# Kernel optimization log

Measured on AMD Instinct MI355X. Metric: run time of the kernel, lower is better.

## Reference

```python
import jax, jax.numpy as jnp
import numpy as np

B, N, C, H, P = 8, 4096, 256, 4, 64  # batch, tokens, hidden, heads, proj_size


def setup_inputs() -> dict:
    key = jax.random.key(0)
    ks = jax.random.split(key, 6)
    sc = 0.02
    x = jax.random.normal(ks[0], (B, N, C), jnp.float32)
    bank = jax.random.normal(ks[1], (B, N, C), jnp.float32)  # unused by forward, kept for fidelity
    W_qkvv = jax.random.normal(ks[2], (4 * C, C), jnp.float32) * sc  # Linear(C, 4C), no bias
    W_E = jax.random.normal(ks[3], (P, N), jnp.float32) * sc          # E = F shared Linear(N, P)
    b_E = jnp.zeros((P,), jnp.float32)
    temperature = jnp.ones((H, 1, 1), jnp.float32)
    temperature2 = jnp.ones((H, 1, 1), jnp.float32)
    W_out1 = jax.random.normal(ks[4], (C // 2, C), jnp.float32) * sc  # out_proj (spatial branch)
    b_out1 = jnp.zeros((C // 2,), jnp.float32)
    W_out2 = jax.random.normal(ks[5], (C // 2, C), jnp.float32) * sc  # out_proj2 (channel branch)
    b_out2 = jnp.zeros((C // 2,), jnp.float32)
    prelu_a = jnp.array(0.25, jnp.float32)  # nn.PReLU() default: single shared slope
    return {"x": x, "bank": bank, "W_qkvv": W_qkvv, "W_E": W_E, "b_E": b_E,
            "temperature": temperature, "temperature2": temperature2,
            "W_out1": W_out1, "b_out1": b_out1, "W_out2": W_out2, "b_out2": b_out2,
            "prelu_a": prelu_a}


def _l2norm(t):
    # torch F.normalize(dim=-1): x / max(||x||_2, eps)
    return t / jnp.maximum(jnp.linalg.norm(t, axis=-1, keepdims=True), 1e-12)


def reference(x, bank, W_qkvv, W_E, b_E, temperature, temperature2,
              W_out1, b_out1, W_out2, b_out2, prelu_a):
    Bb, Nn, Cc = x.shape
    Hh = temperature.shape[0]
    d = Cc // Hh
    # qkvv projection -> [4, B, H, N, d], then transpose token/feature axes -> [B, H, d, N]
    qkvv = (x @ W_qkvv.T).reshape(Bb, Nn, 4, Hh, d).transpose(2, 0, 3, 1, 4)
    q, k, v_ca, v_sa = (qkvv[0].transpose(0, 1, 3, 2), qkvv[1].transpose(0, 1, 3, 2),
                        qkvv[2].transpose(0, 1, 3, 2), qkvv[3].transpose(0, 1, 3, 2))
    # shared linear E=F projects the token axis N -> P (applied to UNnormalized k, v_sa)
    k_proj = jnp.einsum('bhdn,pn->bhdp', k, W_E) + b_E      # [B,H,d,P]
    v_sa_proj = jnp.einsum('bhdn,pn->bhdp', v_sa, W_E) + b_E  # [B,H,d,P]
    qn = _l2norm(q)
    kn = _l2norm(k)
    # channel attention: [B,H,d,d]
    attn_ca = jax.nn.softmax(jnp.einsum('bhdn,bhen->bhde', qn, kn) * temperature, axis=-1)
    x_ca = jnp.einsum('bhde,bhen->bhdn', attn_ca, v_ca).transpose(0, 3, 1, 2).reshape(Bb, Nn, Cc)
    # spatial attention (projected): [B,H,N,P]
    attn_sa = jax.nn.softmax(jnp.einsum('bhdn,bhdp->bhnp', qn, k_proj) * temperature2, axis=-1)
    x_sa = jnp.einsum('bhnp,bhdp->bhnd', attn_sa, v_sa_proj).transpose(0, 2, 1, 3).reshape(Bb, Nn, Cc)
    x_sa = x_sa @ W_out1.T + b_out1
    x_ca = x_ca @ W_out2.T + b_out2
    out = jnp.concatenate([x_sa, x_ca], axis=-1)
    return jnp.where(out >= 0, out, prelu_a * out)  # PReLU
```

## Files before the change

kernel.cpp:

```cpp
#include <hip/hip_runtime.h>
#include <cstdint>
#include <cstddef>

constexpr int B_ = 8, N_ = 4096, C_ = 256, H_ = 4, D_ = 64, P_ = 64;
constexpr int OC_ = 4 * C_;
constexpr int M_  = B_ * N_;
constexpr int GX_ROWS = 320;
constexpr int KS_G = 8;
constexpr int XT_TILES = M_ / 64;

#define DEV_INLINE __device__ __forceinline__

typedef unsigned short ushort_t;
typedef __attribute__((ext_vector_type(8))) short short8;
typedef __attribute__((ext_vector_type(4))) short short4v;
typedef __attribute__((ext_vector_type(4))) float floatx4;

DEV_INLINE short f2bf(float f) {
  unsigned int u = __builtin_bit_cast(unsigned int, f);
  u += 0x7FFFu + ((u >> 16) & 1u);
  return (short)(u >> 16);
}
DEV_INLINE float bf2f(ushort_t u) {
  return __builtin_bit_cast(float, (unsigned int)u << 16);
}
DEV_INLINE short4v cvt4(float4 v) {
  short4v s = {f2bf(v.x), f2bf(v.y), f2bf(v.z), f2bf(v.w)};
  return s;
}

__global__ __launch_bounds__(256) void k_cast(const float* __restrict__ x,
                                              const float* __restrict__ Wq,
                                              const float* __restrict__ WE,
                                              const float* __restrict__ W1,
                                              const float* __restrict__ W2,
                                              ushort_t* __restrict__ xt,
                                              ushort_t* __restrict__ wqb,
                                              ushort_t* __restrict__ web,
                                              ushort_t* __restrict__ w1b,
                                              ushort_t* __restrict__ w2b,
                                              ushort_t* __restrict__ wqtq,
                                              ushort_t* __restrict__ wv2t) {
  __shared__ __align__(16) short Xs[64 * 264];
  const int t = threadIdx.x;
  if (blockIdx.x >= XT_TILES + 128) {
    const int tb = blockIdx.x - (XT_TILES + 128);
    const int srcbase = (tb < 4 ? 0 : 512) + (tb & 3) * 64;
    ushort_t* dstm = (tb < 4) ? wqtq : wv2t;
    const int R = (tb & 3) * 64;
#pragma unroll
    for (int rep = 0; rep < 16; ++rep) {
      const int f4 = rep * 256 + t;
      const int row = f4 >> 6, c4 = f4 & 63;
      float4 v = *(const float4*)&Wq[(size_t)(srcbase + row) * 256 + c4 * 4];
      *(short4v*)&Xs[row * 264 + c4 * 4] = cvt4(v);
    }
    __syncthreads();
    const int ch = t;
    ushort_t* dst = &dstm[ch * 256 + R];
#pragma unroll
    for (int g = 0; g < 8; ++g) {
      short8 o;
#pragma unroll
      for (int i = 0; i < 8; ++i) o[i] = Xs[(g * 8 + i) * 264 + ch];
      *(short8*)&dst[g * 8] = o;
    }
    return;
  }
  if (blockIdx.x >= XT_TILES) {
    constexpr size_t WQ4 = (size_t)OC_ * C_ / 4;
    constexpr size_t WE4 = (size_t)P_ * N_ / 4;
    constexpr size_t W14 = (size_t)128 * C_ / 4;
    constexpr size_t TOTW4 = WQ4 + WE4 + 2 * W14;
    const size_t stride = (size_t)128 * 256;
    for (size_t i = (size_t)(blockIdx.x - XT_TILES) * 256 + t; i < TOTW4; i += stride) {
      const float* src; ushort_t* dst; size_t o;
      if (i < WQ4) { src = Wq; dst = wqb; o = i; }
      else if (i < WQ4 + WE4) { src = WE; dst = web; o = i - WQ4; }
      else if (i < WQ4 + WE4 + W14) { src = W1; dst = w1b; o = i - WQ4 - WE4; }
      else { src = W2; dst = w2b; o = i - WQ4 - WE4 - W14; }
      float4 v = ((const float4*)src)[o];
      *(short4v*)&dst[o * 4] = cvt4(v);
    }
    return;
  }
  const int n0 = blockIdx.x * 64;
  const int b = n0 >> 12, nl = n0 & 4095;
#pragma unroll
  for (int rep = 0; rep < 16; ++rep) {
    const int f4 = rep * 256 + t;
    const int row = f4 >> 6, c4 = f4 & 63;
    float4 v = *(const float4*)&x[(size_t)(n0 + row) * 256 + c4 * 4];
    *(short4v*)&Xs[row * 264 + c4 * 4] = cvt4(v);
  }
  __syncthreads();
  const int ch = t;
  ushort_t* dst = &xt[((size_t)b * 256 + ch) * 4096 + nl];
#pragma unroll
  for (int g = 0; g < 8; ++g) {
    short8 o;
#pragma unroll
    for (int i = 0; i < 8; ++i) o[i] = Xs[(g * 8 + i) * 264 + ch];
    *(short8*)&dst[g * 8] = o;
  }
}

__global__ __launch_bounds__(512) void k_gram(const ushort_t* __restrict__ xt,
                                              const ushort_t* __restrict__ web,
                                              float* __restrict__ Gxp) {
  __shared__ __align__(16) short As[128 * 72];
  __shared__ __align__(16) short Bs[256 * 72];
  const int job = blockIdx.x;
  const int y = blockIdx.y;
  const int b = y >> 3, ksp = y & 7;
  const int t = threadIdx.x;
  const int oc = t & 7, rr = t >> 3;
  const int lane = t & 63, wave = t >> 6;
  const int m16 = lane & 15, quad = lane >> 4;
  const int wm = (wave >> 2) << 6, wn = (wave & 3) << 6;
  const ushort_t* Asrc = (job < 2)
      ? xt + (size_t)(b * 256 + job * 128) * 4096 : web;
  const ushort_t* Bsrc = xt + (size_t)b * 256 * 4096;
  floatx4 acc[4][4];
#pragma unroll
  for (int i = 0; i < 4; ++i)
#pragma unroll
    for (int j = 0; j < 4; ++j) acc[i][j] = (floatx4)(0.f);
#pragma unroll 1
  for (int it = 0; it < 8; ++it) {
    const int n0 = ksp * 512 + it * 64;
    short8 a8[2], b8[4];
#pragma unroll
    for (int rp = 0; rp < 2; ++rp) {
      int ar = rr + 64 * rp;
      if (job == 2) ar &= 63;
      a8[rp] = *(const short8*)&Asrc[(size_t)ar * 4096 + n0 + 8 * oc];
    }
#pragma unroll
    for (int rp = 0; rp < 4; ++rp)
      b8[rp] = *(const short8*)&Bsrc[(size_t)(rr + 64 * rp) * 4096 + n0 + 8 * oc];
    __syncthreads();
#pragma unroll
    for (int rp = 0; rp < 2; ++rp)
      *(short8*)&As[(rr + 64 * rp) * 72 + 8 * oc] = a8[rp];
#pragma unroll
    for (int rp = 0; rp < 4; ++rp)
      *(short8*)&Bs[(rr + 64 * rp) * 72 + 8 * oc] = b8[rp];
    __syncthreads();
#pragma unroll
    for (int ks = 0; ks < 2; ++ks) {
      if (job < 2) {
        short8 af[4], bf[4];
#pragma unroll
        for (int i = 0; i < 4; ++i)
          af[i] = *(const short8*)&As[(wm + i * 16 + m16) * 72 + ks * 32 + quad * 8];
#pragma unroll
        for (int j = 0; j < 4; ++j)
          bf[j] = *(const short8*)&Bs[(wn + j * 16 + m16) * 72 + ks * 32 + quad * 8];
#pragma unroll
        for (int i = 0; i < 4; ++i)
#pragma unroll
          for (int j = 0; j < 4; ++j)
            acc[i][j] = __builtin_amdgcn_mfma_f32_16x16x32_bf16(af[i], bf[j], acc[i][j], 0, 0, 0);
      } else {
        short8 af[4], bf[2];
#pragma unroll
        for (int i = 0; i < 4; ++i)
          af[i] = *(const short8*)&As[(i * 16 + m16) * 72 + ks * 32 + quad * 8];
#pragma unroll
        for (int j = 0; j < 2; ++j)
          bf[j] = *(const short8*)&Bs[(wave * 32 + j * 16 + m16) * 72 + ks * 32 + quad * 8];
#pragma unroll
        for (int i = 0; i < 4; ++i)
#pragma unroll
          for (int j = 0; j < 2; ++j)
            acc[i][j] = __builtin_amdgcn_mfma_f32_16x16x32_bf16(af[i], bf[j], acc[i][j], 0, 0, 0);
      }
    }
  }
  float* pb = Gxp + (size_t)y * (GX_ROWS * 256);
  if (job < 2) {
#pragma unroll
    for (int i = 0; i < 4; ++i)
#pragma unroll
      for (int r = 0; r < 4; ++r) {
        const int grow = job * 128 + wm + i * 16 + quad * 4 + r;
#pragma unroll
        for (int j = 0; j < 4; ++j)
          pb[(size_t)grow * 256 + wn + j * 16 + m16] = acc[i][j][r];
      }
  } else {
#pragma unroll
    for (int i = 0; i < 4; ++i)
#pragma unroll
      for (int r = 0; r < 4; ++r) {
        const int grow = 256 + i * 16 + quad * 4 + r;
#pragma unroll
        for (int j = 0; j < 2; ++j)
          pb[(size_t)grow * 256 + wave * 32 + j * 16 + m16] = acc[i][j][r];
      }
  }
}

__global__ __launch_bounds__(256) void k_gred(const float* __restrict__ Gxp,
                                              float* __restrict__ Gx) {
  const int i = blockIdx.x * 256 + threadIdx.x;
  constexpr int PB4 = GX_ROWS * 256 / 4;
  const int fb = i / PB4, rem = i - fb * PB4;
  const float4* p = (const float4*)Gxp;
  float4 s = p[(size_t)fb * KS_G * PB4 + rem];
#pragma unroll
  for (int k = 1; k < KS_G; ++k) {
    float4 v = p[((size_t)fb * KS_G + k) * PB4 + rem];
    s.x += v.x; s.y += v.y; s.z += v.z; s.w += v.w;
  }
  ((float4*)Gx)[i] = s;
}

__global__ __launch_bounds__(256) void k_mid1(const ushort_t* __restrict__ wqb,
                                              const float* __restrict__ Gx,
                                              ushort_t* __restrict__ T2b,
                                              float* __restrict__ ssq) {
  __shared__ __align__(16) short As[128 * 72];
  __shared__ __align__(16) short Bs[128 * 72];
  const int bm = blockIdx.x * 128;
  const int b  = blockIdx.y >> 1;
  const int jb = blockIdx.y & 1;
  const int t = threadIdx.x;
  const int oc = t & 7;
  const int rr = t >> 3;
  const int lane = t & 63, wave = t >> 6;
  const int m16 = lane & 15, quad = lane >> 4;
  const int wm = (wave >> 1) << 6, wn = (wave & 1) << 6;
  const float* Bsrc = Gx + ((size_t)b * GX_ROWS + jb * 128) * 256;
  floatx4 acc[4][4];
#pragma unroll
  for (int i = 0; i < 4; ++i)
#pragma unroll
    for (int j = 0; j < 4; ++j) acc[i][j] = (floatx4)(0.f);
#pragma unroll 1
  for (int k0 = 0; k0 < 256; k0 += 64) {
    short8 a8[4], b8[4];
#pragma unroll
    for (int j = 0; j < 4; ++j) {
      const int r = rr + 32 * j;
      a8[j] = *(const short8*)&wqb[(size_t)(bm + r) * 256 + k0 + 8 * oc];
      float4 g0 = *(const float4*)&Bsrc[(size_t)r * 256 + k0 + 8 * oc];
      float4 g1 = *(const float4*)&Bsrc[(size_t)r * 256 + k0 + 8 * oc + 4];
      short8 bb;
      bb[0] = f2bf(g0.x); bb[1] = f2bf(g0.y); bb[2] = f2bf(g0.z); bb[3] = f2bf(g0.w);
      bb[4] = f2bf(g1.x); bb[5] = f2bf(g1.y); bb[6] = f2bf(g1.z); bb[7] = f2bf(g1.w);
      b8[j] = bb;
    }
    __syncthreads();
#pragma unroll
    for (int j = 0; j < 4; ++j) {
      const int r = rr + 32 * j;
      *(short8*)&As[r * 72 + 8 * oc] = a8[j];
      *(short8*)&Bs[r * 72 + 8 * oc] = b8[j];
    }
    __syncthreads();
#pragma unroll
    for (int ks = 0; ks < 2; ++ks) {
      short8 af[4], bf[4];
#pragma unroll
      for (int i = 0; i < 4; ++i)
        af[i] = *(const short8*)&As[(wm + i * 16 + m16) * 72 + ks * 32 + quad * 8];
#pragma unroll
      for (int j = 0; j < 4; ++j)
        bf[j] = *(const short8*)&Bs[(wn + j * 16 + m16) * 72 + ks * 32 + quad * 8];
#pragma unroll
      for (int i = 0; i < 4; ++i)
#pragma unroll
        for (int j = 0; j < 4; ++j)
          acc[i][j] = __builtin_amdgcn_mfma_f32_16x16x32_bf16(af[i], bf[j], acc[i][j], 0, 0, 0);
    }
  }
#pragma unroll
  for (int i = 0; i < 4; ++i)
#pragma unroll
    for (int r = 0; r < 4; ++r) {
      const int gr = bm + wm + i * 16 + quad * 4 + r;
      float s = 0.f;
#pragma unroll
      for (int j = 0; j < 4; ++j) {
        const int col = jb * 128 + wn + j * 16 + m16;
        T2b[((size_t)b * 512 + gr) * 256 + col] = (ushort_t)f2bf(acc[i][j][r]);
        s += bf2f(wqb[(size_t)gr * 256 + col]) * acc[i][j][r];
      }
      s += __shfl_xor(s, 1);
      s += __shfl_xor(s, 2);
      s += __shfl_xor(s, 4);
      s += __shfl_xor(s, 8);
      if (m16 == 0) atomicAdd(&ssq[b * 512 + gr], s);
    }
}

__global__ __launch_bounds__(256) void k_mid2(const ushort_t* __restrict__ wqb,
                                              const ushort_t* __restrict__ T2b,
                                              const float* __restrict__ Gx,
                                              const float* __restrict__ ssq,
                                              const float* __restrict__ bE,
                                              const float* __restrict__ t1,
                                              const float* __restrict__ t2,
                                              ushort_t* __restrict__ ab,
                                              ushort_t* __restrict__ ksb,
                                              ushort_t* __restrict__ vsb) {
  const int bh = blockIdx.x;
  const int job = blockIdx.y;
  const int b = bh >> 2, h = bh & 3;
  const int wave = threadIdx.x >> 6;
  const int lane = threadIdx.x & 63;
  const int m16 = lane & 15, quad = lane >> 4;
  const int Abase = (job == 0 ? 0 : (job == 1 ? 256 : 768)) + h * 64;
  const int arow = Abase + 16 * wave + m16;
  floatx4 acc[4];
#pragma unroll
  for (int j = 0; j < 4; ++j) acc[j] = (floatx4)(0.f);
#pragma unroll
  for (int ks = 0; ks < 8; ++ks) {
    const int boct = ks * 32 + quad * 8;
    short8 af = *(const short8*)&wqb[(size_t)arow * 256 + boct];
    short8 bf[4];
    if (job == 0) {
#pragma unroll
      for (int j = 0; j < 4; ++j)
        bf[j] = *(const short8*)&T2b[((size_t)b * 512 + 256 + h * 64 + 16 * j + m16) * 256 + boct];
    } else {
#pragma unroll
      for (int j = 0; j < 4; ++j) {
        const float* gp = Gx + ((size_t)b * GX_ROWS + 256 + 16 * j + m16) * 256 + boct;
        float4 g0 = *(const float4*)gp;
        float4 g1 = *(const float4*)(gp + 4);
        short8 bb;
        bb[0] = f2bf(g0.x); bb[1] = f2bf(g0.y); bb[2] = f2bf(g0.z); bb[3] = f2bf(g0.w);
        bb[4] = f2bf(g1.x); bb[5] = f2bf(g1.y); bb[6] = f2bf(g1.z); bb[7] = f2bf(g1.w);
        bf[j] = bb;
      }
    }
#pragma unroll
    for (int j = 0; j < 4; ++j)
      acc[j] = __builtin_amdgcn_mfma_f32_16x16x32_bf16(af, bf[j], acc[j], 0, 0, 0);
  }
  if (job == 0) {
    const float t1h = t1[h];
    float rnk[4];
#pragma unroll
    for (int j = 0; j < 4; ++j)
      rnk[j] = 1.f / fmaxf(sqrtf(ssq[b * 512 + 256 + h * 64 + 16 * j + m16]), 1e-12f);
#pragma unroll
    for (int r = 0; r < 4; ++r) {
      const int d = 16 * wave + quad * 4 + r;
      const float rq = 1.f / fmaxf(sqrtf(ssq[b * 512 + h * 64 + d]), 1e-12f);
      float l[4];
      float m = -1e30f;
#pragma unroll
      for (int j = 0; j < 4; ++j) {
        l[j] = acc[j][r] * rq * rnk[j] * t1h;
        m = fmaxf(m, l[j]);
      }
      m = fmaxf(m, __shfl_xor(m, 1));
      m = fmaxf(m, __shfl_xor(m, 2));
      m = fmaxf(m, __shfl_xor(m, 4));
      m = fmaxf(m, __shfl_xor(m, 8));
      float s = 0.f;
#pragma unroll
      for (int j = 0; j < 4; ++j) {
        l[j] = __expf(l[j] - m);
        s += l[j];
      }
      s += __shfl_xor(s, 1);
      s += __shfl_xor(s, 2);
      s += __shfl_xor(s, 4);
      s += __shfl_xor(s, 8);
      const float inv = 1.f / s;
#pragma unroll
      for (int j = 0; j < 4; ++j)
        ab[(size_t)bh * 4096 + d * 64 + 16 * j + m16] = (ushort_t)f2bf(l[j] * inv);
    }
  } else if (job == 1) {
    const float tt = t2[h];
#pragma unroll
    for (int r = 0; r < 4; ++r) {
      const int d = 16 * wave + quad * 4 + r;
      const float rq = 1.f / fmaxf(sqrtf(ssq[b * 512 + h * 64 + d]), 1e-12f);
#pragma unroll
      for (int j = 0; j < 4; ++j) {
        const int p = 16 * j + m16;
        ksb[(size_t)bh * 4096 + p * 64 + d] =
            (ushort_t)f2bf((acc[j][r] + bE[p]) * rq * tt);
      }
    }
  } else {
#pragma unroll
    for (int r = 0; r < 4; ++r) {
      const int d = 16 * wave + quad * 4 + r;
#pragma unroll
      for (int j = 0; j < 4; ++j) {
        const int p = 16 * j + m16;
        vsb[(size_t)bh * 4096 + d * 64 + p] = (ushort_t)f2bf(acc[j][r] + bE[p]);
      }
    }
  }
}

__global__ __launch_bounds__(256) void k_mid3(const ushort_t* __restrict__ ksb,
                                              const ushort_t* __restrict__ ab,
                                              const ushort_t* __restrict__ wqtq,
                                              const ushort_t* __restrict__ wv2t,
                                              ushort_t* __restrict__ Kc,
                                              ushort_t* __restrict__ AcT) {
  const int bh = blockIdx.x;
  const int job = blockIdx.y;
  const int h = bh & 3;
  const int wave = threadIdx.x >> 6;
  const int lane = threadIdx.x & 63;
  const int m16 = lane & 15, quad = lane >> 4;
  const ushort_t* A = (job ? ab : ksb) + (size_t)bh * 4096;
  const ushort_t* Bt = job ? wv2t : wqtq;
  floatx4 acc[4][4];
#pragma unroll
  for (int i = 0; i < 4; ++i)
#pragma unroll
    for (int j = 0; j < 4; ++j) acc[i][j] = (floatx4)(0.f);
#pragma unroll
  for (int ks = 0; ks < 2; ++ks) {
    const int boct = ks * 32 + quad * 8;
    short8 af[4], bf[4];
#pragma unroll
    for (int i = 0; i < 4; ++i)
      af[i] = *(const short8*)&A[(16 * i + m16) * 64 + boct];
#pragma unroll
    for (int j = 0; j < 4; ++j)
      bf[j] = *(const short8*)&Bt[(size_t)(wave * 64 + 16 * j + m16) * 256 + h * 64 + boct];
#pragma unroll
    for (int i = 0; i < 4; ++i)
#pragma unroll
      for (int j = 0; j < 4; ++j)
        acc[i][j] = __builtin_amdgcn_mfma_f32_16x16x32_bf16(af[i], bf[j], acc[i][j], 0, 0, 0);
  }
#pragma unroll
  for (int i = 0; i < 4; ++i)
#pragma unroll
    for (int r = 0; r < 4; ++r) {
      const int ar = 16 * i + quad * 4 + r;
#pragma unroll
      for (int j = 0; j < 4; ++j) {
        const int cc = wave * 64 + 16 * j + m16;
        if (job == 0)
          Kc[(size_t)bh * 16384 + ar * 256 + cc] = (ushort_t)f2bf(acc[i][j][r]);
        else
          AcT[(size_t)bh * 16384 + cc * 64 + ar] = (ushort_t)f2bf(acc[i][j][r]);
      }
    }
}

__global__ __launch_bounds__(256) void k_mid4(const ushort_t* __restrict__ w2b,
                                              const ushort_t* __restrict__ AcT,
                                              ushort_t* __restrict__ M2) {
  const int b = blockIdx.x;
  const int ob = blockIdx.y * 64;
  const int wave = threadIdx.x >> 6;
  const int lane = threadIdx.x & 63;
  const int m16 = lane & 15, quad = lane >> 4;
  floatx4 acc[4][4];
#pragma unroll
  for (int i = 0; i < 4; ++i)
#pragma unroll
    for (int j = 0; j < 4; ++j) acc[i][j] = (floatx4)(0.f);
#pragma unroll
  for (int ks = 0; ks < 8; ++ks) {
    const int boct = ks * 32 + quad * 8;
    const int hsel = boct >> 6, de = boct & 63;
    short8 af[4], bf[4];
#pragma unroll
    for (int i = 0; i < 4; ++i)
      af[i] = *(const short8*)&w2b[(size_t)(ob + 16 * i + m16) * 256 + boct];
#pragma unroll
    for (int j = 0; j < 4; ++j)
      bf[j] = *(const short8*)&AcT[((size_t)(b * 4 + hsel)) * 16384 +
                                   (wave * 64 + 16 * j + m16) * 64 + de];
#pragma unroll
    for (int i = 0; i < 4; ++i)
#pragma unroll
      for (int j = 0; j < 4; ++j)
        acc[i][j] = __builtin_amdgcn_mfma_f32_16x16x32_bf16(af[i], bf[j], acc[i][j], 0, 0, 0);
  }
#pragma unroll
  for (int i = 0; i < 4; ++i)
#pragma unroll
    for (int r = 0; r < 4; ++r) {
      const int oo = ob + 16 * i + quad * 4 + r;
#pragma unroll
      for (int j = 0; j < 4; ++j)
        M2[(size_t)b * 32768 + oo * 256 + wave * 64 + 16 * j + m16] =
            (ushort_t)f2bf(acc[i][j][r]);
    }
}

__global__ __launch_bounds__(256, 2) void k_tok(const float* __restrict__ x,
                                                const ushort_t* __restrict__ Kc,
                                                const ushort_t* __restrict__ vsb,
                                                const ushort_t* __restrict__ M2,
                                                const ushort_t* __restrict__ w1b,
                                                const float* __restrict__ b1,
                                                const float* __restrict__ b2,
                                                const float* __restrict__ pa,
                                                float* __restrict__ out) {
  __shared__ __align__(16) short Xs[64 * 264];
  __shared__ __align__(16) short Ys[64 * 264];
  const int n0 = blockIdx.x * 64;
  const int b = n0 >> 12;
  const int t = threadIdx.x;
  const int lane = t & 63, wave = t >> 6;
  const int m16 = lane & 15, quad = lane >> 4;
  const int cw = wave * 64;
  const int bh = b * 4 + wave;
#pragma unroll
  for (int rep = 0; rep < 16; ++rep) {
    const int f4 = rep * 256 + t;
    const int row = f4 >> 6, c4 = f4 & 63;
    float4 v = *(const float4*)&x[(size_t)(n0 + row) * 256 + c4 * 4];
    *(short4v*)&Xs[row * 264 + c4 * 4] = cvt4(v);
  }
  __syncthreads();
  {
    floatx4 s[4][4];
#pragma unroll
    for (int i = 0; i < 4; ++i)
#pragma unroll
      for (int j = 0; j < 4; ++j) s[i][j] = (floatx4)(0.f);
#pragma unroll
    for (int ks = 0; ks < 8; ++ks) {
      const int boct = ks * 32 + quad * 8;
      short8 af[4], bf[4];
#pragma unroll
      for (int i = 0; i < 4; ++i)
        af[i] = *(const short8*)&Xs[(16 * i + m16) * 264 + boct];
#pragma unroll
      for (int j = 0; j < 4; ++j)
        bf[j] = *(const short8*)&Kc[(size_t)bh * 16384 + (16 * j + m16) * 256 + boct];
#pragma unroll
      for (int i = 0; i < 4; ++i)
#pragma unroll
        for (int j = 0; j < 4; ++j)
          s[i][j] = __builtin_amdgcn_mfma_f32_16x16x32_bf16(af[i], bf[j], s[i][j], 0, 0, 0);
    }
#pragma unroll
    for (int i = 0; i < 4; ++i)
#pragma unroll
      for (int r = 0; r < 4; ++r) {
        float mr = fmaxf(fmaxf(s[i][0][r], s[i][1][r]), fmaxf(s[i][2][r], s[i][3][r]));
        mr = fmaxf(mr, __shfl_xor(mr, 1));
        mr = fmaxf(mr, __shfl_xor(mr, 2));
        mr = fmaxf(mr, __shfl_xor(mr, 4));
        mr = fmaxf(mr, __shfl_xor(mr, 8));
        float sr = 0.f;
#pragma unroll
        for (int j = 0; j < 4; ++j) {
          const float e = __expf(s[i][j][r] - mr);
          s[i][j][r] = e;
          sr += e;
        }
        sr += __shfl_xor(sr, 1);
        sr += __shfl_xor(sr, 2);
        sr += __shfl_xor(sr, 4);
        sr += __shfl_xor(sr, 8);
        const float inv = 1.f / sr;
#pragma unroll
        for (int j = 0; j < 4; ++j) s[i][j][r] *= inv;
      }
#pragma unroll
    for (int i = 0; i < 4; ++i)
#pragma unroll
      for (int r = 0; r < 4; ++r)
#pragma unroll
        for (int j = 0; j < 4; ++j)
          Ys[(16 * i + quad * 4 + r) * 264 + cw + 16 * j + m16] =
              (short)f2bf(s[i][j][r]);
  }
  {
    floatx4 o[4][4];
#pragma unroll
    for (int i = 0; i < 4; ++i)
#pragma unroll
      for (int j = 0; j < 4; ++j) o[i][j] = (floatx4)(0.f);
#pragma unroll
    for (int ks = 0; ks < 2; ++ks) {
      const int boct = ks * 32 + quad * 8;
      short8 af[4], bf[4];
#pragma unroll
      for (int i = 0; i < 4; ++i)
        af[i] = *(const short8*)&Ys[(16 * i + m16) * 264 + cw + boct];
#pragma unroll
      for (int j = 0; j < 4; ++j)
        bf[j] = *(const short8*)&vsb[(size_t)bh * 4096 + (16 * j + m16) * 64 + boct];
#pragma unroll
      for (int i = 0; i < 4; ++i)
#pragma unroll
        for (int j = 0; j < 4; ++j)
          o[i][j] = __builtin_amdgcn_mfma_f32_16x16x32_bf16(af[i], bf[j], o[i][j], 0, 0, 0);
    }
#pragma unroll
    for (int i = 0; i < 4; ++i)
#pragma unroll
      for (int r = 0; r < 4; ++r)
#pragma unroll
        for (int j = 0; j < 4; ++j)
          Ys[(16 * i + quad * 4 + r) * 264 + cw + 16 * j + m16] =
              (short)f2bf(o[i][j][r]);
  }
  __syncthreads();
  {
    const short* Asrc = (wave < 2) ? Ys : Xs;
    const ushort_t* Wsrc = (wave < 2) ? w1b : (M2 + (size_t)b * 32768);
    const float* bias = (wave < 2) ? b1 : b2;
    const int wrow = (wave & 1) * 64;
    const int colbase = (wave < 2 ? 0 : 128) + wrow;
    floatx4 acc[4][4];
#pragma unroll
    for (int i = 0; i < 4; ++i)
#pragma unroll
      for (int j = 0; j < 4; ++j) acc[i][j] = (floatx4)(0.f);
#pragma unroll
    for (int ks = 0; ks < 8; ++ks) {
      const int boct = ks * 32 + quad * 8;
      short8 af[4], bf[4];
#pragma unroll
      for (int i = 0; i < 4; ++i)
        af[i] = *(const short8*)&Asrc[(16 * i + m16) * 264 + boct];
#pragma unroll
      for (int j = 0; j < 4; ++j)
        bf[j] = *(const short8*)&Wsrc[(size_t)(wrow + 16 * j + m16) * 256 + boct];
#pragma unroll
      for (int i = 0; i < 4; ++i)
#pragma unroll
        for (int j = 0; j < 4; ++j)
          acc[i][j] = __builtin_amdgcn_mfma_f32_16x16x32_bf16(af[i], bf[j], acc[i][j], 0, 0, 0);
    }
    const float slope = pa[0];
    float bj[4];
#pragma unroll
    for (int j = 0; j < 4; ++j) bj[j] = bias[wrow + 16 * j + m16];
#pragma unroll
    for (int i = 0; i < 4; ++i)
#pragma unroll
      for (int r = 0; r < 4; ++r) {
        const int gr = n0 + 16 * i + quad * 4 + r;
#pragma unroll
        for (int j = 0; j < 4; ++j) {
          float v = acc[i][j][r] + bj[j];
          v = v >= 0.f ? v : slope * v;
          out[(size_t)gr * C_ + colbase + 16 * j + m16] = v;
        }
      }
  }
}

extern "C" void kernel_launch(void* const* d_in, const int* in_sizes, int n_in,
                              void* d_out, int out_size, void* d_ws, size_t ws_size,
                              hipStream_t stream) {
  (void)in_sizes; (void)n_in; (void)out_size; (void)ws_size;
  const float* x  = (const float*)d_in[0];
  const float* Wq = (const float*)d_in[2];
  const float* WE = (const float*)d_in[3];
  const float* bE = (const float*)d_in[4];
  const float* t1 = (const float*)d_in[5];
  const float* t2 = (const float*)d_in[6];
  const float* W1 = (const float*)d_in[7];
  const float* b1 = (const float*)d_in[8];
  const float* W2 = (const float*)d_in[9];
  const float* b2 = (const float*)d_in[10];
  const float* pa = (const float*)d_in[11];
  float* out = (float*)d_out;

  float* ws = (float*)d_ws;
  size_t off = 0;
  float* Gx  = ws + off; off += (size_t)B_ * GX_ROWS * 256;
  float* ssq = ws + off; off += (size_t)B_ * 512;
  float* Gxp = ws + off; off += (size_t)KS_G * B_ * GX_ROWS * 256;
  ushort_t* ksb = (ushort_t*)(ws + off); off += 32 * 4096 / 2;
  ushort_t* vsb = (ushort_t*)(ws + off); off += 32 * 4096 / 2;
  ushort_t* ab  = (ushort_t*)(ws + off); off += 32 * 4096 / 2;
  ushort_t* xt  = (ushort_t*)(ws + off); off += (size_t)M_ * C_ / 2;
  ushort_t* wqb = (ushort_t*)(ws + off); off += (size_t)OC_ * C_ / 2;
  ushort_t* w1b = (ushort_t*)(ws + off); off += (size_t)128 * C_ / 2;
  ushort_t* w2b = (ushort_t*)(ws + off); off += (size_t)128 * C_ / 2;
  ushort_t* web = (ushort_t*)(ws + off); off += (size_t)P_ * N_ / 2;
  ushort_t* T2b = (ushort_t*)(ws + off); off += (size_t)B_ * 512 * C_ / 2;
  ushort_t* wqtq = (ushort_t*)(ws + off); off += (size_t)256 * 256 / 2;
  ushort_t* wv2t = (ushort_t*)(ws + off); off += (size_t)256 * 256 / 2;
  ushort_t* Kc  = (ushort_t*)(ws + off); off += (size_t)32 * 16384 / 2;
  ushort_t* AcT = (ushort_t*)(ws + off); off += (size_t)32 * 16384 / 2;
  ushort_t* M2  = (ushort_t*)(ws + off); off += (size_t)B_ * 32768 / 2;

  hipMemsetAsync(ssq, 0, (size_t)B_ * 512 * sizeof(float), stream);

  k_cast<<<XT_TILES + 136, 256, 0, stream>>>(x, Wq, WE, W1, W2,
                                             xt, wqb, web, w1b, w2b, wqtq, wv2t);
  k_gram<<<dim3(3, B_ * KS_G), 512, 0, stream>>>(xt, web, Gxp);
  k_gred<<<GX_ROWS * 256 * B_ / 4 / 256, 256, 0, stream>>>(Gxp, Gx);
  k_mid1<<<dim3(4, B_ * 2), 256, 0, stream>>>(wqb, Gx, T2b, ssq);
  k_mid2<<<dim3(32, 3), 256, 0, stream>>>(wqb, T2b, Gx, ssq, bE, t1, t2, ab, ksb, vsb);
  k_mid3<<<dim3(32, 2), 256, 0, stream>>>(ksb, ab, wqtq, wv2t, Kc, AcT);
  k_mid4<<<dim3(8, 2), 256, 0, stream>>>(w2b, AcT, M2);
  k_tok<<<M_ / 64, 256, 0, stream>>>(x, Kc, vsb, M2, w1b, b1, b2, pa, out);
}
```

Before: 226.8 us.

## Fuse mid2 and mid3 kernels via shared memory and fold ssq zeroing into cast

Merges the per-head softmax/projection kernel with the following small GEMM kernel, so the attention matrix and scaled k-projection stay in LDS instead of going through global memory, and one launch is removed. The ssq memset is also folded into the first block of the cast kernel, removing a separate memset call. The cost is that the fused kernel runs on only 32 blocks doing the three jobs serially, where the old launches spread them over 96 and 64 blocks, so per-block latency goes up.

```diff
diff --git a/kernel.cpp b/kernel.cpp
--- a/kernel.cpp
+++ b/kernel.cpp
@@ -40,9 +40,13 @@
                                               ushort_t* __restrict__ w1b,
                                               ushort_t* __restrict__ w2b,
                                               ushort_t* __restrict__ wqtq,
-                                              ushort_t* __restrict__ wv2t) {
+                                              ushort_t* __restrict__ wv2t,
+                                              float* __restrict__ ssq) {
   __shared__ __align__(16) short Xs[64 * 264];
   const int t = threadIdx.x;
+  if (blockIdx.x == 0) {
+    for (int i = t; i < B_ * 512; i += 256) ssq[i] = 0.f;
+  }
   if (blockIdx.x >= XT_TILES + 128) {
     const int tb = blockIdx.x - (XT_TILES + 128);
     const int srcbase = (tb < 4 ? 0 : 512) + (tb & 3) * 64;
@@ -303,30 +307,81 @@
                                               const float* __restrict__ bE,
                                               const float* __restrict__ t1,
                                               const float* __restrict__ t2,
-                                              ushort_t* __restrict__ ab,
-                                              ushort_t* __restrict__ ksb,
-                                              ushort_t* __restrict__ vsb) {
+                                              const ushort_t* __restrict__ wqtq,
+                                              const ushort_t* __restrict__ wv2t,
+                                              ushort_t* __restrict__ vsb,
+                                              ushort_t* __restrict__ Kc,
+                                              ushort_t* __restrict__ AcT) {
+  __shared__ __align__(16) short Ab[64 * 64];
+  __shared__ __align__(16) short Kb[64 * 64];
   const int bh = blockIdx.x;
-  const int job = blockIdx.y;
   const int b = bh >> 2, h = bh & 3;
   const int wave = threadIdx.x >> 6;
   const int lane = threadIdx.x & 63;
   const int m16 = lane & 15, quad = lane >> 4;
-  const int Abase = (job == 0 ? 0 : (job == 1 ? 256 : 768)) + h * 64;
-  const int arow = Abase + 16 * wave + m16;
-  floatx4 acc[4];
-#pragma unroll
-  for (int j = 0; j < 4; ++j) acc[j] = (floatx4)(0.f);
-#pragma unroll
-  for (int ks = 0; ks < 8; ++ks) {
-    const int boct = ks * 32 + quad * 8;
-    short8 af = *(const short8*)&wqb[(size_t)arow * 256 + boct];
-    short8 bf[4];
-    if (job == 0) {
+  {
+    const int arow = h * 64 + 16 * wave + m16;
+    floatx4 acc[4];
+#pragma unroll
+    for (int j = 0; j < 4; ++j) acc[j] = (floatx4)(0.f);
+#pragma unroll
+    for (int ks = 0; ks < 8; ++ks) {
+      const int boct = ks * 32 + quad * 8;
+      short8 af = *(const short8*)&wqb[(size_t)arow * 256 + boct];
+      short8 bf[4];
 #pragma unroll
       for (int j = 0; j < 4; ++j)
         bf[j] = *(const short8*)&T2b[((size_t)b * 512 + 256 + h * 64 + 16 * j + m16) * 256 + boct];
-    } else {
+#pragma unroll
+      for (int j = 0; j < 4; ++j)
+        acc[j] = __builtin_amdgcn_mfma_f32_16x16x32_bf16(af, bf[j], acc[j], 0, 0, 0);
+    }
+    const float t1h = t1[h];
+    float rnk[4];
+#pragma unroll
+    for (int j = 0; j < 4; ++j)
+      rnk[j] = 1.f / fmaxf(sqrtf(ssq[b * 512 + 256 + h * 64 + 16 * j + m16]), 1e-12f);
+#pragma unroll
+    for (int r = 0; r < 4; ++r) {
+      const int d = 16 * wave + quad * 4 + r;
+      const float rq = 1.f / fmaxf(sqrtf(ssq[b * 512 + h * 64 + d]), 1e-12f);
+      float l[4];
+      float m = -1e30f;
+#pragma unroll
+      for (int j = 0; j < 4; ++j) {
+        l[j] = acc[j][r] * rq * rnk[j] * t1h;
+        m = fmaxf(m, l[j]);
+      }
+      m = fmaxf(m, __shfl_xor(m, 1));
+      m = fmaxf(m, __shfl_xor(m, 2));
+      m = fmaxf(m, __shfl_xor(m, 4));
+      m = fmaxf(m, __shfl_xor(m, 8));
+      float s = 0.f;
+#pragma unroll
+      for (int j = 0; j < 4; ++j) {
+        l[j] = __expf(l[j] - m);
+        s += l[j];
+      }
+      s += __shfl_xor(s, 1);
+      s += __shfl_xor(s, 2);
+      s += __shfl_xor(s, 4);
+      s += __shfl_xor(s, 8);
+      const float inv = 1.f / s;
+#pragma unroll
+      for (int j = 0; j < 4; ++j)
+        Ab[d * 64 + 16 * j + m16] = (short)f2bf(l[j] * inv);
+    }
+  }
+  {
+    const int arow = 256 + h * 64 + 16 * wave + m16;
+    floatx4 acc[4];
+#pragma unroll
+    for (int j = 0; j < 4; ++j) acc[j] = (floatx4)(0.f);
+#pragma unroll
+    for (int ks = 0; ks < 8; ++ks) {
+      const int boct = ks * 32 + quad * 8;
+      short8 af = *(const short8*)&wqb[(size_t)arow * 256 + boct];
+      short8 bf[4];
 #pragma unroll
       for (int j = 0; j < 4; ++j) {
         const float* gp = Gx + ((size_t)b * GX_ROWS + 256 + 16 * j + m16) * 256 + boct;
@@ -337,61 +392,46 @@
         bb[4] = f2bf(g1.x); bb[5] = f2bf(g1.y); bb[6] = f2bf(g1.z); bb[7] = f2bf(g1.w);
         bf[j] = bb;
       }
-    }
-#pragma unroll
-    for (int j = 0; j < 4; ++j)
-      acc[j] = __builtin_amdgcn_mfma_f32_16x16x32_bf16(af, bf[j], acc[j], 0, 0, 0);
-  }
-  if (job == 0) {
-    const float t1h = t1[h];
-    float rnk[4];
-#pragma unroll
-    for (int j = 0; j < 4; ++j)
-      rnk[j] = 1.f / fmaxf(sqrtf(ssq[b * 512 + 256 + h * 64 + 16 * j + m16]), 1e-12f);
+#pragma unroll
+      for (int j = 0; j < 4; ++j)
+        acc[j] = __builtin_amdgcn_mfma_f32_16x16x32_bf16(af, bf[j], acc[j], 0, 0, 0);
+    }
+    const float tt = t2[h];
 #pragma unroll
     for (int r = 0; r < 4; ++r) {
       const int d = 16 * wave + quad * 4 + r;
       const float rq = 1.f / fmaxf(sqrtf(ssq[b * 512 + h * 64 + d]), 1e-12f);
-      float l[4];
-      float m = -1e30f;
-#pragma unroll
-      for (int j = 0; j < 4; ++j) {
-        l[j] = acc[j][r] * rq * rnk[j] * t1h;
-        m = fmaxf(m, l[j]);
-      }
-      m = fmaxf(m, __shfl_xor(m, 1));
-      m = fmaxf(m, __shfl_xor(m, 2));
-      m = fmaxf(m, __shfl_xor(m, 4));
-      m = fmaxf(m, __shfl_xor(m, 8));
-      float s = 0.f;
-#pragma unroll
-      for (int j = 0; j < 4; ++j) {
-        l[j] = __expf(l[j] - m);
-        s += l[j];
-      }
-      s += __shfl_xor(s, 1);
-      s += __shfl_xor(s, 2);
-      s += __shfl_xor(s, 4);
-      s += __shfl_xor(s, 8);
-      const float inv = 1.f / s;
-#pragma unroll
-      for (int j = 0; j < 4; ++j)
-        ab[(size_t)bh * 4096 + d * 64 + 16 * j + m16] = (ushort_t)f2bf(l[j] * inv);
-    }
-  } else if (job == 1) {
-    const float tt = t2[h];
-#pragma unroll
-    for (int r = 0; r < 4; ++r) {
-      const int d = 16 * wave + quad * 4 + r;
-      const float rq = 1.f / fmaxf(sqrtf(ssq[b * 512 + h * 64 + d]), 1e-12f);
 #pragma unroll
       for (int j = 0; j < 4; ++j) {
         const int p = 16 * j + m16;
-        ksb[(size_t)bh * 4096 + p * 64 + d] =
-            (ushort_t)f2bf((acc[j][r] + bE[p]) * rq * tt);
-      }
-    }
-  } else {
+        Kb[p * 64 + d] = (short)f2bf((acc[j][r] + bE[p]) * rq * tt);
+      }
+    }
+  }
+  {
+    const int arow = 768 + h * 64 + 16 * wave + m16;
+    floatx4 acc[4];
+#pragma unroll
+    for (int j = 0; j < 4; ++j) acc[j] = (floatx4)(0.f);
+#pragma unroll
+    for (int ks = 0; ks < 8; ++ks) {
+      const int boct = ks * 32 + quad * 8;
+      short8 af = *(const short8*)&wqb[(size_t)arow * 256 + boct];
+      short8 bf[4];
+#pragma unroll
+      for (int j = 0; j < 4; ++j) {
+        const float* gp = Gx + ((size_t)b * GX_ROWS + 256 + 16 * j + m16) * 256 + boct;
+        float4 g0 = *(const float4*)gp;
+        float4 g1 = *(const float4*)(gp + 4);
+        short8 bb;
+        bb[0] = f2bf(g0.x); bb[1] = f2bf(g0.y); bb[2] = f2bf(g0.z); bb[3] = f2bf(g0.w);
+        bb[4] = f2bf(g1.x); bb[5] = f2bf(g1.y); bb[6] = f2bf(g1.z); bb[7] = f2bf(g1.w);
+        bf[j] = bb;
+      }
+#pragma unroll
+      for (int j = 0; j < 4; ++j)
+        acc[j] = __builtin_amdgcn_mfma_f32_16x16x32_bf16(af, bf[j], acc[j], 0, 0, 0);
+    }
 #pragma unroll
     for (int r = 0; r < 4; ++r) {
       const int d = 16 * wave + quad * 4 + r;
@@ -402,57 +442,75 @@
       }
     }
   }
-}
-
-__global__ __launch_bounds__(256) void k_mid3(const ushort_t* __restrict__ ksb,
-                                              const ushort_t* __restrict__ ab,
-                                              const ushort_t* __restrict__ wqtq,
-                                              const ushort_t* __restrict__ wv2t,
-                                              ushort_t* __restrict__ Kc,
-                                              ushort_t* __restrict__ AcT) {
-  const int bh = blockIdx.x;
-  const int job = blockIdx.y;
-  const int h = bh & 3;
-  const int wave = threadIdx.x >> 6;
-  const int lane = threadIdx.x & 63;
-  const int m16 = lane & 15, quad = lane >> 4;
-  const ushort_t* A = (job ? ab : ksb) + (size_t)bh * 4096;
-  const ushort_t* Bt = job ? wv2t : wqtq;
-  floatx4 acc[4][4];
-#pragma unroll
-  for (int i = 0; i < 4; ++i)
-#pragma unroll
-    for (int j = 0; j < 4; ++j) acc[i][j] = (floatx4)(0.f);
-#pragma unroll
-  for (int ks = 0; ks < 2; ++ks) {
-    const int boct = ks * 32 + quad * 8;
-    short8 af[4], bf[4];
-#pragma unroll
-    for (int i = 0; i < 4; ++i)
-      af[i] = *(const short8*)&A[(16 * i + m16) * 64 + boct];
-#pragma unroll
-    for (int j = 0; j < 4; ++j)
-      bf[j] = *(const short8*)&Bt[(size_t)(wave * 64 + 16 * j + m16) * 256 + h * 64 + boct];
-#pragma unroll
-    for (int i = 0; i < 4; ++i)
-#pragma unroll
-      for (int j = 0; j < 4; ++j)
-        acc[i][j] = __builtin_amdgcn_mfma_f32_16x16x32_bf16(af[i], bf[j], acc[i][j], 0, 0, 0);
-  }
-#pragma unroll
-  for (int i = 0; i < 4; ++i)
-#pragma unroll
-    for (int r = 0; r < 4; ++r) {
-      const int ar = 16 * i + quad * 4 + r;
-#pragma unroll
-      for (int j = 0; j < 4; ++j) {
-        const int cc = wave * 64 + 16 * j + m16;
-        if (job == 0)
-          Kc[(size_t)bh * 16384 + ar * 256 + cc] = (ushort_t)f2bf(acc[i][j][r]);
-        else
-          AcT[(size_t)bh * 16384 + cc * 64 + ar] = (ushort_t)f2bf(acc[i][j][r]);
-      }
-    }
+  __syncthreads();
+  {
+    floatx4 acc[4][4];
+#pragma unroll
+    for (int i = 0; i < 4; ++i)
+#pragma unroll
+      for (int j = 0; j < 4; ++j) acc[i][j] = (floatx4)(0.f);
+#pragma unroll
+    for (int ks = 0; ks < 2; ++ks) {
+      const int boct = ks * 32 + quad * 8;
+      short8 af[4], bf[4];
+#pragma unroll
+      for (int i = 0; i < 4; ++i)
+        af[i] = *(const short8*)&Kb[(16 * i + m16) * 64 + boct];
+#pragma unroll
+      for (int j = 0; j < 4; ++j)
+        bf[j] = *(const short8*)&wqtq[(size_t)(wave * 64 + 16 * j + m16) * 256 + h * 64 + boct];
+#pragma unroll
+      for (int i = 0; i < 4; ++i)
+#pragma unroll
+        for (int j = 0; j < 4; ++j)
+          acc[i][j] = __builtin_amdgcn_mfma_f32_16x16x32_bf16(af[i], bf[j], acc[i][j], 0, 0, 0);
+    }
+#pragma unroll
+    for (int i = 0; i < 4; ++i)
+#pragma unroll
+      for (int r = 0; r < 4; ++r) {
+        const int p = 16 * i + quad * 4 + r;
+#pragma unroll
+        for (int j = 0; j < 4; ++j) {
+          const int cc = wave * 64 + 16 * j + m16;
+          Kc[(size_t)bh * 16384 + p * 256 + cc] = (ushort_t)f2bf(acc[i][j][r]);
+        }
+      }
+  }
+  {
+    floatx4 acc[4][4];
+#pragma unroll
+    for (int i = 0; i < 4; ++i)
+#pragma unroll
+      for (int j = 0; j < 4; ++j) acc[i][j] = (floatx4)(0.f);
+#pragma unroll
+    for (int ks = 0; ks < 2; ++ks) {
+      const int boct = ks * 32 + quad * 8;
+      short8 af[4], bf[4];
+#pragma unroll
+      for (int i = 0; i < 4; ++i)
+        af[i] = *(const short8*)&Ab[(16 * i + m16) * 64 + boct];
+#pragma unroll
+      for (int j = 0; j < 4; ++j)
+        bf[j] = *(const short8*)&wv2t[(size_t)(wave * 64 + 16 * j + m16) * 256 + h * 64 + boct];
+#pragma unroll
+      for (int i = 0; i < 4; ++i)
+#pragma unroll
+        for (int j = 0; j < 4; ++j)
+          acc[i][j] = __builtin_amdgcn_mfma_f32_16x16x32_bf16(af[i], bf[j], acc[i][j], 0, 0, 0);
+    }
+#pragma unroll
+    for (int i = 0; i < 4; ++i)
+#pragma unroll
+      for (int r = 0; r < 4; ++r) {
+        const int dd = 16 * i + quad * 4 + r;
+#pragma unroll
+        for (int j = 0; j < 4; ++j) {
+          const int cc = wave * 64 + 16 * j + m16;
+          AcT[(size_t)bh * 16384 + cc * 64 + dd] = (ushort_t)f2bf(acc[i][j][r]);
+        }
+      }
+  }
 }
 
 __global__ __launch_bounds__(256) void k_mid4(const ushort_t* __restrict__ w2b,
@@ -679,9 +737,7 @@
   float* Gx  = ws + off; off += (size_t)B_ * GX_ROWS * 256;
   float* ssq = ws + off; off += (size_t)B_ * 512;
   float* Gxp = ws + off; off += (size_t)KS_G * B_ * GX_ROWS * 256;
-  ushort_t* ksb = (ushort_t*)(ws + off); off += 32 * 4096 / 2;
   ushort_t* vsb = (ushort_t*)(ws + off); off += 32 * 4096 / 2;
-  ushort_t* ab  = (ushort_t*)(ws + off); off += 32 * 4096 / 2;
   ushort_t* xt  = (ushort_t*)(ws + off); off += (size_t)M_ * C_ / 2;
   ushort_t* wqb = (ushort_t*)(ws + off); off += (size_t)OC_ * C_ / 2;
   ushort_t* w1b = (ushort_t*)(ws + off); off += (size_t)128 * C_ / 2;
@@ -694,15 +750,13 @@
   ushort_t* AcT = (ushort_t*)(ws + off); off += (size_t)32 * 16384 / 2;
   ushort_t* M2  = (ushort_t*)(ws + off); off += (size_t)B_ * 32768 / 2;
 
-  hipMemsetAsync(ssq, 0, (size_t)B_ * 512 * sizeof(float), stream);
-
   k_cast<<<XT_TILES + 136, 256, 0, stream>>>(x, Wq, WE, W1, W2,
-                                             xt, wqb, web, w1b, w2b, wqtq, wv2t);
+                                             xt, wqb, web, w1b, w2b, wqtq, wv2t, ssq);
   k_gram<<<dim3(3, B_ * KS_G), 512, 0, stream>>>(xt, web, Gxp);
   k_gred<<<GX_ROWS * 256 * B_ / 4 / 256, 256, 0, stream>>>(Gxp, Gx);
   k_mid1<<<dim3(4, B_ * 2), 256, 0, stream>>>(wqb, Gx, T2b, ssq);
-  k_mid2<<<dim3(32, 3), 256, 0, stream>>>(wqb, T2b, Gx, ssq, bE, t1, t2, ab, ksb, vsb);
-  k_mid3<<<dim3(32, 2), 256, 0, stream>>>(ksb, ab, wqtq, wv2t, Kc, AcT);
+  k_mid2<<<32, 256, 0, stream>>>(wqb, T2b, Gx, ssq, bE, t1, t2,
+                                 wqtq, wv2t, vsb, Kc, AcT);
   k_mid4<<<dim3(8, 2), 256, 0, stream>>>(w2b, AcT, M2);
   k_tok<<<M_ / 64, 256, 0, stream>>>(x, Kc, vsb, M2, w1b, b1, b2, pa, out);
 }
```

After: 241.1 us. +6.3%, slower.
